# Performance work log

Hardware: AMD Instinct MI355X
Metric: run time of the kernel (lower is better)

Reference implementation:

```python
import jax, jax.numpy as jnp
import numpy as np

# LAB normalization constants (Zhang et al. colorization convention used in this repo)
L_CENT, L_NORM, AB_NORM = 50.0, 100.0, 110.0
_RGB2XYZ = np.array([[0.412453, 0.357580, 0.180423],
                     [0.212671, 0.715160, 0.072169],
                     [0.019334, 0.119193, 0.950227]], dtype=np.float32)
_XYZ_WHITE = np.array([0.95047, 1.0, 1.08883], dtype=np.float32)


def rgb2lab(rgb):
    """rgb: (B,3,H,W) in [-0.5,0.5] -> normalized LAB (B,3,H,W)."""
    rgb01 = rgb + 0.5  # [0,1]
    # sRGB gamma expansion (safe-where for grad stability)
    m = rgb01 > 0.04045
    rgb_safe = jnp.where(m, rgb01, 1.0)
    lin = jnp.where(m, ((rgb_safe + 0.055) / 1.055) ** 2.4, rgb01 / 12.92)
    xyz = jnp.einsum('ij,bjhw->bihw', jnp.asarray(_RGB2XYZ), lin)
    xyz = xyz / jnp.asarray(_XYZ_WHITE)[None, :, None, None]
    m2 = xyz > 0.008856
    xyz_safe = jnp.where(m2, xyz, 1.0)
    f = jnp.where(m2, xyz_safe ** (1.0 / 3.0), 7.787 * xyz + 16.0 / 116.0)
    L = 116.0 * f[:, 1] - 16.0
    a = 500.0 * (f[:, 0] - f[:, 1])
    b = 200.0 * (f[:, 1] - f[:, 2])
    return jnp.stack([(L - L_CENT) / L_NORM, a / AB_NORM, b / AB_NORM], axis=1)


def setup_inputs() -> dict:
    key = jax.random.key(0)
    k0, k1, k2, k3 = jax.random.split(key, 4)
    B, C, H, W, F = 2, 3, 64, 64, 64
    rgb0 = jax.random.uniform(k0, (B, C, H, W), dtype=jnp.float32) - 0.5
    rgb1 = jax.random.uniform(k1, (B, C, H, W), dtype=jnp.float32) - 0.5
    feat0 = jax.random.normal(k2, (B, F, H, W), dtype=jnp.float32)
    feat1 = jax.random.normal(k3, (B, F, H, W), dtype=jnp.float32)
    return {"rgb0": rgb0, "rgb1": rgb1, "feat0": feat0, "feat1": feat1}


def reference(rgb0, rgb1, feat0, feat1):
    l1_coeff, huber_coeff = 1.0, 1.0  # hyp.col2D_l1_coeff / hyp.col2D_huber_coeff
    B, C, H, W = rgb0.shape
    F = feat0.shape[1]
    N = H * W
    lab0 = rgb2lab(rgb0)
    lab1 = rgb2lab(rgb1)
    f0 = feat0.reshape(B, F, N)
    f1 = feat1.reshape(B, F, N)
    corr = jnp.einsum('bfn,bfm->bnm', f0, f1) / 0.07  # (B,N,N)
    att = jax.nn.softmax(corr, axis=2)
    lab1_flat = lab1.reshape(B, C, N)
    # broadcast-multiply-sum in the original == attention @ labels (same math)
    lab0_e = jnp.einsum('bnm,bcm->bcn', att, lab1_flat).reshape(B, C, H, W)
    diff = lab0_e - lab0
    l1_loss = jnp.mean(jnp.sum(jnp.abs(diff), axis=1, keepdims=True))
    ad = jnp.abs(diff)
    huber = jnp.where(ad < 1.0, 0.5 * ad * ad, ad - 0.5)  # SmoothL1, beta=1
    huber_loss = jnp.mean(jnp.sum(huber, axis=1, keepdims=True))
    total_loss = l1_coeff * l1_loss + huber_coeff * huber_loss
    return total_loss
```

## Files before the change

kernel.cpp:

```cpp
#include <hip/hip_runtime.h>
#include <math.h>

#define NPIX   4096
#define FDIM   64
#define BATCH  2
#define SPLIT  8
#define CHUNK  (NPIX / SPLIT)
#define NGROUP (CHUNK / 64)

typedef __attribute__((ext_vector_type(8))) short short8;
typedef __attribute__((ext_vector_type(4))) float floatx4;

__device__ __forceinline__ float exp2f_(float x) { return __builtin_amdgcn_exp2f(x); }

__device__ __forceinline__ short f2bf(float x) {
    union { float f; unsigned u; } c; c.f = x;
    unsigned r = (c.u + 0x7FFFu + ((c.u >> 16) & 1u)) >> 16;
    return (short)r;
}

__device__ __forceinline__ float gamma_expand(float u) {
    return u > 0.04045f ? powf((u + 0.055f) * (1.0f / 1.055f), 2.4f)
                        : u * (1.0f / 12.92f);
}
__device__ __forceinline__ float lab_f(float t) {
    return t > 0.008856f ? cbrtf(t) : 7.787f * t + (16.0f / 116.0f);
}

__global__ __launch_bounds__(256) void prep_kernel(
    const float* __restrict__ rgb0, const float* __restrict__ rgb1,
    const float* __restrict__ feat0, const float* __restrict__ feat1,
    float* __restrict__ lab0, float* __restrict__ lab1,
    short* __restrict__ f0t, short* __restrict__ f1t)
{
    int bid = blockIdx.x;
    int tid = threadIdx.x;

    if (bid < 256) {
        __shared__ short Tsm[64 * 72];
        int pair = bid >> 6;
        int tensor = pair >> 1;
        int bb = pair & 1;
        int n0 = (bid & 63) * 64;
        const float* src = (tensor ? feat1 : feat0) + (size_t)bb * FDIM * NPIX;
        short* dst = (tensor ? f1t : f0t) + (size_t)bb * NPIX * FDIM;
        float scale = tensor ? 1.0f : (1.442695040888963f / 0.07f);

        int f = tid >> 2;
        int slot = tid & 3;
        #pragma unroll
        for (int i = 0; i < 4; ++i) {
            int col4 = slot * 4 + i;
            int noff = col4 * 4;
            float4 v = *(const float4*)&src[(size_t)f * NPIX + n0 + noff];
            Tsm[(noff + 0) * 72 + f] = f2bf(v.x * scale);
            Tsm[(noff + 1) * 72 + f] = f2bf(v.y * scale);
            Tsm[(noff + 2) * 72 + f] = f2bf(v.z * scale);
            Tsm[(noff + 3) * 72 + f] = f2bf(v.w * scale);
        }
        __syncthreads();
        #pragma unroll
        for (int i = 0; i < 2; ++i) {
            int idx = i * 256 + tid;
            int row = idx >> 3, ch = idx & 7;
            *(short8*)&dst[(size_t)(n0 + row) * FDIM + ch * 8] =
                *(const short8*)&Tsm[row * 72 + ch * 8];
        }
        return;
    }

    int gid = (bid - 256) * 256 + tid;
    int img = gid / (BATCH * NPIX);
    int rem = gid - img * (BATCH * NPIX);
    int b = rem / NPIX;
    int n = rem - b * NPIX;
    const float* rgb = img ? rgb1 : rgb0;
    float* lab = img ? lab1 : lab0;

    size_t i0 = (size_t)(b * 3 + 0) * NPIX + n;
    size_t i1 = (size_t)(b * 3 + 1) * NPIX + n;
    size_t i2 = (size_t)(b * 3 + 2) * NPIX + n;

    float r = gamma_expand(rgb[i0] + 0.5f);
    float g = gamma_expand(rgb[i1] + 0.5f);
    float bl = gamma_expand(rgb[i2] + 0.5f);

    float X = (0.412453f * r + 0.357580f * g + 0.180423f * bl) * (1.0f / 0.95047f);
    float Y = (0.212671f * r + 0.715160f * g + 0.072169f * bl);
    float Z = (0.019334f * r + 0.119193f * g + 0.950227f * bl) * (1.0f / 1.08883f);

    float fx = lab_f(X), fy = lab_f(Y), fz = lab_f(Z);
    float L = 116.0f * fy - 16.0f;
    float a = 500.0f * (fx - fy);
    float bb2 = 200.0f * (fy - fz);

    lab[i0] = (L - 50.0f) * (1.0f / 100.0f);
    lab[i1] = a * (1.0f / 110.0f);
    lab[i2] = bb2 * (1.0f / 110.0f);
}

__global__ __launch_bounds__(256, 4) void attn_kernel(
    const short* __restrict__ f0t, const short* __restrict__ f1t,
    const float* __restrict__ lab1ws, float* __restrict__ partials)
{
    __shared__ short Bsm[64 * 72];
    __shared__ float Lt[3 * 64];

    int bid = blockIdx.x;
    int rowblk = bid & 63;
    int chunk = (bid >> 6) & 7;
    int b = bid >> 9;
    int n0 = rowblk * 64;
    int m_base = chunk * CHUNK;

    int tid = threadIdx.x;
    int w = tid >> 6;
    int l = tid & 63;
    int c = l & 15;
    int q = l >> 4;

    const short8* aptr = (const short8*)(f0t +
        ((size_t)b * NPIX + n0 + w * 16 + c) * FDIM + q * 8);
    short8 a0 = aptr[0];
    short8 a1 = aptr[4];

    float m_st[4], sum_st[4], s0_st[4], s1_st[4], s2_st[4];
    #pragma unroll
    for (int r = 0; r < 4; ++r) {
        m_st[r] = -INFINITY; sum_st[r] = 0.0f;
        s0_st[r] = 0.0f; s1_st[r] = 0.0f; s2_st[r] = 0.0f;
    }

    for (int g = 0; g < NGROUP; ++g) {
        int m0 = m_base + g * 64;
        __syncthreads();
        #pragma unroll
        for (int i = 0; i < 2; ++i) {
            int idx = i * 256 + tid;
            int row = idx >> 3, ch = idx & 7;
            *(short8*)&Bsm[row * 72 + ch * 8] =
                *(const short8*)&f1t[((size_t)b * NPIX + m0 + row) * FDIM + ch * 8];
        }
        if (tid < 48) {
            int cc = tid >> 4, m4 = tid & 15;
            *(float4*)&Lt[cc * 64 + m4 * 4] =
                *(const float4*)&lab1ws[(size_t)(b * 3 + cc) * NPIX + m0 + m4 * 4];
        }
        __syncthreads();

        floatx4 acc[4];
        #pragma unroll
        for (int t = 0; t < 4; ++t) acc[t] = (floatx4)(0.0f);

        #pragma unroll
        for (int t = 0; t < 4; ++t) {
            const short8* bp = (const short8*)&Bsm[(t * 16 + c) * 72 + q * 8];
            short8 b0 = bp[0];
            short8 b1 = bp[4];
            acc[t] = __builtin_amdgcn_mfma_f32_16x16x32_bf16(a0, b0, acc[t], 0, 0, 0);
            acc[t] = __builtin_amdgcn_mfma_f32_16x16x32_bf16(a1, b1, acc[t], 0, 0, 0);
        }

        float lA[4], lB[4], lC[4];
        #pragma unroll
        for (int t = 0; t < 4; ++t) {
            lA[t] = Lt[0 * 64 + t * 16 + c];
            lB[t] = Lt[1 * 64 + t * 16 + c];
            lC[t] = Lt[2 * 64 + t * 16 + c];
        }

        #pragma unroll
        for (int r = 0; r < 4; ++r) {
            float L0 = acc[0][r], L1 = acc[1][r], L2 = acc[2][r], L3 = acc[3][r];
            float tmax = fmaxf(fmaxf(L0, L1), fmaxf(L2, L3));
            float nm = fmaxf(m_st[r], tmax);
            float sc = exp2f_(m_st[r] - nm);
            float p0 = exp2f_(L0 - nm);
            float p1 = exp2f_(L1 - nm);
            float p2 = exp2f_(L2 - nm);
            float p3 = exp2f_(L3 - nm);
            sum_st[r] = sum_st[r] * sc + ((p0 + p1) + (p2 + p3));
            s0_st[r] = s0_st[r] * sc + ((p0 * lA[0] + p1 * lA[1]) + (p2 * lA[2] + p3 * lA[3]));
            s1_st[r] = s1_st[r] * sc + ((p0 * lB[0] + p1 * lB[1]) + (p2 * lB[2] + p3 * lB[3]));
            s2_st[r] = s2_st[r] * sc + ((p0 * lC[0] + p1 * lC[1]) + (p2 * lC[2] + p3 * lC[3]));
            m_st[r] = nm;
        }
    }

    #pragma unroll
    for (int mask = 1; mask <= 8; mask <<= 1) {
        #pragma unroll
        for (int r = 0; r < 4; ++r) {
            float om = __shfl_xor(m_st[r], mask, 64);
            float os = __shfl_xor(sum_st[r], mask, 64);
            float o0 = __shfl_xor(s0_st[r], mask, 64);
            float o1 = __shfl_xor(s1_st[r], mask, 64);
            float o2 = __shfl_xor(s2_st[r], mask, 64);
            float nm = fmaxf(m_st[r], om);
            float w1 = exp2f_(m_st[r] - nm);
            float w2 = exp2f_(om - nm);
            sum_st[r] = sum_st[r] * w1 + os * w2;
            s0_st[r] = s0_st[r] * w1 + o0 * w2;
            s1_st[r] = s1_st[r] * w1 + o1 * w2;
            s2_st[r] = s2_st[r] * w1 + o2 * w2;
            m_st[r] = nm;
        }
    }

    if (c == 0) {
        #pragma unroll
        for (int r = 0; r < 4; ++r) {
            int row_g = n0 + w * 16 + q * 4 + r;
            size_t base = (size_t)(b * SPLIT + chunk) * 5 * NPIX + row_g;
            partials[base + 0 * NPIX] = m_st[r];
            partials[base + 1 * NPIX] = sum_st[r];
            partials[base + 2 * NPIX] = s0_st[r];
            partials[base + 3 * NPIX] = s1_st[r];
            partials[base + 4 * NPIX] = s2_st[r];
        }
    }
}

__global__ void loss_kernel(const float* __restrict__ partials,
                            const float* __restrict__ lab0ws,
                            float* __restrict__ out)
{
    int gid = blockIdx.x * blockDim.x + threadIdx.x;
    int b = gid >> 12;
    int n = gid & (NPIX - 1);

    float mc[SPLIT];
    float M = -INFINITY;
    #pragma unroll
    for (int ch = 0; ch < SPLIT; ++ch) {
        mc[ch] = partials[((size_t)(b * SPLIT + ch) * 5 + 0) * NPIX + n];
        M = fmaxf(M, mc[ch]);
    }
    float S = 0.0f, A0 = 0.0f, A1 = 0.0f, A2 = 0.0f;
    #pragma unroll
    for (int ch = 0; ch < SPLIT; ++ch) {
        size_t base = (size_t)(b * SPLIT + ch) * 5 * NPIX + n;
        float w = exp2f_(mc[ch] - M);
        S  += partials[base + 1 * NPIX] * w;
        A0 += partials[base + 2 * NPIX] * w;
        A1 += partials[base + 3 * NPIX] * w;
        A2 += partials[base + 4 * NPIX] * w;
    }
    float inv_s = 1.0f / S;
    float d0 = A0 * inv_s - lab0ws[(size_t)(b * 3 + 0) * NPIX + n];
    float d1 = A1 * inv_s - lab0ws[(size_t)(b * 3 + 1) * NPIX + n];
    float d2 = A2 * inv_s - lab0ws[(size_t)(b * 3 + 2) * NPIX + n];

    float val = 0.0f;
    #pragma unroll
    for (int cc = 0; cc < 3; ++cc) {
        float d = (cc == 0) ? d0 : (cc == 1) ? d1 : d2;
        float ad = fabsf(d);
        float hub = (ad < 1.0f) ? 0.5f * ad * ad : ad - 0.5f;
        val += ad + hub;
    }

    #pragma unroll
    for (int off = 32; off > 0; off >>= 1)
        val += __shfl_down(val, off);

    __shared__ float wsum[4];
    int lane = threadIdx.x & 63;
    int wave = threadIdx.x >> 6;
    if (lane == 0) wsum[wave] = val;
    __syncthreads();
    if (threadIdx.x == 0) {
        float s = wsum[0] + wsum[1] + wsum[2] + wsum[3];
        atomicAdd(out, s * (1.0f / 8192.0f));
    }
}

extern "C" void kernel_launch(void* const* d_in, const int* in_sizes, int n_in,
                              void* d_out, int out_size, void* d_ws, size_t ws_size,
                              hipStream_t stream) {
    const float* rgb0  = (const float*)d_in[0];
    const float* rgb1  = (const float*)d_in[1];
    const float* feat0 = (const float*)d_in[2];
    const float* feat1 = (const float*)d_in[3];
    float* out = (float*)d_out;
    float* ws  = (float*)d_ws;

    float* lab0 = ws;
    float* lab1 = ws + 24576;
    float* partials = ws + 49152;
    short* f0t = (short*)(ws + 376832);
    short* f1t = f0t + (size_t)BATCH * NPIX * FDIM;

    hipMemsetAsync(d_out, 0, sizeof(float), stream);

    prep_kernel<<<320, 256, 0, stream>>>(rgb0, rgb1, feat0, feat1, lab0, lab1, f0t, f1t);

    int attn_grid = BATCH * SPLIT * (NPIX / 64);
    attn_kernel<<<attn_grid, 256, 0, stream>>>(f0t, f1t, lab1, partials);

    loss_kernel<<<(BATCH * NPIX) / 256, 256, 0, stream>>>(partials, lab0, out);
}
```

Measured before the change: 89.12 us.

## Load key tiles directly from global, preload label chunk, double split count

The attention kernel no longer stages each key tile through shared memory with two barriers per group. Each lane now reads its B fragments straight from global/L2, and the lab1 chunk is preloaded into LDS once. SPLIT rises from 8 to 16, doubling the grid to improve occupancy, and the output memset is folded into the prep kernel, removing one launch. In exchange, the loss kernel must merge twice as many partials, and repeated global reads of the key tiles lean on cache hits.

```diff
diff --git a/kernel.cpp b/kernel.cpp
--- a/kernel.cpp
+++ b/kernel.cpp
@@ -4,7 +4,7 @@
 #define NPIX   4096
 #define FDIM   64
 #define BATCH  2
-#define SPLIT  8
+#define SPLIT  16
 #define CHUNK  (NPIX / SPLIT)
 #define NGROUP (CHUNK / 64)
 
@@ -31,7 +31,8 @@
     const float* __restrict__ rgb0, const float* __restrict__ rgb1,
     const float* __restrict__ feat0, const float* __restrict__ feat1,
     float* __restrict__ lab0, float* __restrict__ lab1,
-    short* __restrict__ f0t, short* __restrict__ f1t)
+    short* __restrict__ f0t, short* __restrict__ f1t,
+    float* __restrict__ out)
 {
     int bid = blockIdx.x;
     int tid = threadIdx.x;
@@ -69,6 +70,8 @@
         return;
     }
 
+    if (bid == 256 && tid == 0) out[0] = 0.0f;
+
     int gid = (bid - 256) * 256 + tid;
     int img = gid / (BATCH * NPIX);
     int rem = gid - img * (BATCH * NPIX);
@@ -103,13 +106,12 @@
     const short* __restrict__ f0t, const short* __restrict__ f1t,
     const float* __restrict__ lab1ws, float* __restrict__ partials)
 {
-    __shared__ short Bsm[64 * 72];
-    __shared__ float Lt[3 * 64];
+    __shared__ float Lt[3 * CHUNK];
 
     int bid = blockIdx.x;
     int rowblk = bid & 63;
-    int chunk = (bid >> 6) & 7;
-    int b = bid >> 9;
+    int chunk = (bid >> 6) & (SPLIT - 1);
+    int b = bid >> 10;
     int n0 = rowblk * 64;
     int m_base = chunk * CHUNK;
 
@@ -119,11 +121,20 @@
     int c = l & 15;
     int q = l >> 4;
 
+    if (tid < 192) {
+        int cc = tid >> 6;
+        int m4 = tid & 63;
+        *(float4*)&Lt[cc * CHUNK + m4 * 4] =
+            *(const float4*)&lab1ws[(size_t)(b * 3 + cc) * NPIX + m_base + m4 * 4];
+    }
+
     const short8* aptr = (const short8*)(f0t +
         ((size_t)b * NPIX + n0 + w * 16 + c) * FDIM + q * 8);
     short8 a0 = aptr[0];
     short8 a1 = aptr[4];
 
+    __syncthreads();
+
     float m_st[4], sum_st[4], s0_st[4], s1_st[4], s2_st[4];
     #pragma unroll
     for (int r = 0; r < 4; ++r) {
@@ -131,42 +142,29 @@
         s0_st[r] = 0.0f; s1_st[r] = 0.0f; s2_st[r] = 0.0f;
     }
 
+    const short8* bbase = (const short8*)(f1t +
+        ((size_t)b * NPIX + m_base + c) * FDIM + q * 8);
+
+    #pragma unroll
     for (int g = 0; g < NGROUP; ++g) {
-        int m0 = m_base + g * 64;
-        __syncthreads();
-        #pragma unroll
-        for (int i = 0; i < 2; ++i) {
-            int idx = i * 256 + tid;
-            int row = idx >> 3, ch = idx & 7;
-            *(short8*)&Bsm[row * 72 + ch * 8] =
-                *(const short8*)&f1t[((size_t)b * NPIX + m0 + row) * FDIM + ch * 8];
-        }
-        if (tid < 48) {
-            int cc = tid >> 4, m4 = tid & 15;
-            *(float4*)&Lt[cc * 64 + m4 * 4] =
-                *(const float4*)&lab1ws[(size_t)(b * 3 + cc) * NPIX + m0 + m4 * 4];
-        }
-        __syncthreads();
-
         floatx4 acc[4];
         #pragma unroll
-        for (int t = 0; t < 4; ++t) acc[t] = (floatx4)(0.0f);
-
-        #pragma unroll
         for (int t = 0; t < 4; ++t) {
-            const short8* bp = (const short8*)&Bsm[(t * 16 + c) * 72 + q * 8];
+            const short8* bp = bbase + (size_t)(g * 64 + t * 16) * 8;
             short8 b0 = bp[0];
             short8 b1 = bp[4];
-            acc[t] = __builtin_amdgcn_mfma_f32_16x16x32_bf16(a0, b0, acc[t], 0, 0, 0);
+            floatx4 z = (floatx4)(0.0f);
+            acc[t] = __builtin_amdgcn_mfma_f32_16x16x32_bf16(a0, b0, z, 0, 0, 0);
             acc[t] = __builtin_amdgcn_mfma_f32_16x16x32_bf16(a1, b1, acc[t], 0, 0, 0);
         }
 
         float lA[4], lB[4], lC[4];
         #pragma unroll
         for (int t = 0; t < 4; ++t) {
-            lA[t] = Lt[0 * 64 + t * 16 + c];
-            lB[t] = Lt[1 * 64 + t * 16 + c];
-            lC[t] = Lt[2 * 64 + t * 16 + c];
+            int m = g * 64 + t * 16 + c;
+            lA[t] = Lt[0 * CHUNK + m];
+            lB[t] = Lt[1 * CHUNK + m];
+            lC[t] = Lt[2 * CHUNK + m];
         }
 
         #pragma unroll
@@ -229,18 +227,15 @@
     int b = gid >> 12;
     int n = gid & (NPIX - 1);
 
-    float mc[SPLIT];
     float M = -INFINITY;
     #pragma unroll
-    for (int ch = 0; ch < SPLIT; ++ch) {
-        mc[ch] = partials[((size_t)(b * SPLIT + ch) * 5 + 0) * NPIX + n];
-        M = fmaxf(M, mc[ch]);
-    }
+    for (int ch = 0; ch < SPLIT; ++ch)
+        M = fmaxf(M, partials[((size_t)(b * SPLIT + ch) * 5 + 0) * NPIX + n]);
     float S = 0.0f, A0 = 0.0f, A1 = 0.0f, A2 = 0.0f;
     #pragma unroll
     for (int ch = 0; ch < SPLIT; ++ch) {
         size_t base = (size_t)(b * SPLIT + ch) * 5 * NPIX + n;
-        float w = exp2f_(mc[ch] - M);
+        float w = exp2f_(partials[base + 0 * NPIX] - M);
         S  += partials[base + 1 * NPIX] * w;
         A0 += partials[base + 2 * NPIX] * w;
         A1 += partials[base + 3 * NPIX] * w;
@@ -288,12 +283,10 @@
     float* lab0 = ws;
     float* lab1 = ws + 24576;
     float* partials = ws + 49152;
-    short* f0t = (short*)(ws + 376832);
+    short* f0t = (short*)(ws + 49152 + 655360);
     short* f1t = f0t + (size_t)BATCH * NPIX * FDIM;
 
-    hipMemsetAsync(d_out, 0, sizeof(float), stream);
-
-    prep_kernel<<<320, 256, 0, stream>>>(rgb0, rgb1, feat0, feat1, lab0, lab1, f0t, f1t);
+    prep_kernel<<<320, 256, 0, stream>>>(rgb0, rgb1, feat0, feat1, lab0, lab1, f0t, f1t, out);
 
     int attn_grid = BATCH * SPLIT * (NPIX / 64);
     attn_kernel<<<attn_grid, 256, 0, stream>>>(f0t, f1t, lab1, partials);
```

Measured after the change: 106.6 us. 19.6% more time.
